# Kernel tuning notes

Hardware: AMD Instinct MI355X
Metric: run time of the kernel (lower is better)

The kernel has to match this reference:

```python
import jax, jax.numpy as jnp
import numpy as np

IN_CH, OUT_CH, K, STRIDE, PAD = 256, 256, 5, 1, 2


def setup_inputs() -> dict:
    key = jax.random.key(0)
    kx, kw = jax.random.split(key)
    x = jax.random.normal(kx, (32, IN_CH, 4096), dtype=jnp.float32)
    # kaiming_uniform_(a=sqrt(5)) -> bound = 1/sqrt(fan_in), fan_in = in_ch*k
    bound = 1.0 / np.sqrt(IN_CH * K)
    weight = jax.random.uniform(kw, (OUT_CH, IN_CH, K), dtype=jnp.float32,
                                minval=-bound, maxval=bound)
    bias = jnp.zeros((OUT_CH,), dtype=jnp.float32)
    return {"x": x, "weight": weight, "bias": bias}


def reference(x, weight, bias):
    # x: [B, C_in, W]; weight: [C_out, C_in, K] -> out: [B, C_out, W_out]
    out = jax.lax.conv_general_dilated(
        x, weight,
        window_strides=(STRIDE,),
        padding=[(PAD, PAD)],
        dimension_numbers=("NCH", "OIH", "NCH"),
    )
    return out + bias[None, :, None]
```

## Files before the change

kernel.cpp:

```cpp
#include <hip/hip_runtime.h>
#include <hip/hip_bf16.h>

typedef unsigned short u16;
typedef unsigned int u32;
typedef unsigned long long u64;
typedef __attribute__((ext_vector_type(8))) short short8;
typedef __attribute__((ext_vector_type(4))) float floatx4;

#define NB 32
#define NCI 256
#define NCO 256
#define NW 4096
#define NK 5

#define W3ROWB 80
#define W3TILE (256 * W3ROWB)
#define W3_BYTES (40 * W3TILE)

#define XROWB 64
#define XROWS 264
#define XBUF (XROWS * XROWB)

#define XSWZ(row) ((((row) >> 1) & 3) << 4)


__global__ void wprep(const float* __restrict__ wgt, u16* __restrict__ W3) {
    int i = blockIdx.x * 256 + threadIdx.x;
    if (i >= NCO * NCI * NK) return;
    int k  = i % NK;
    int ci = (i / NK) % NCI;
    int co = i / (NCI * NK);
    int cb = ci >> 5, cr = ci & 31;
    __hip_bfloat16 h = __float2bfloat16(wgt[i]);
    W3[((size_t)(cb * NK + k) * 256 + co) * 40 + cr] = *reinterpret_cast<u16*>(&h);
}

__device__ __forceinline__ u16 bf16bits(float f) {
    __hip_bfloat16 h = __float2bfloat16(f);
    return *reinterpret_cast<u16*>(&h);
}


__global__ __launch_bounds__(512, 2)
void conv_mfma(const float* __restrict__ x, const u16* __restrict__ W3,
               const float* __restrict__ bias, float* __restrict__ out) {
    __shared__ __align__(16) char xlds[2 * XBUF];

    const int bid  = blockIdx.x;
    const int wt   = bid & 15;
    const int b    = bid >> 4;
    const int tid  = threadIdx.x;
    const int lane = tid & 63;
    const int wave = tid >> 6;
    const int wm   = wave >> 2;
    const int wn   = wave & 3;
    const int mrow = lane & 15;
    const int g    = lane >> 4;
    const int w0   = wt * 256;

    floatx4 acc[8][4];
#pragma unroll
    for (int mi = 0; mi < 8; ++mi)
#pragma unroll
        for (int ni = 0; ni < 4; ++ni)
            acc[mi][ni] = (floatx4){0.f, 0.f, 0.f, 0.f};

    const float* xb = x + (size_t)b * NCI * NW;

    const int srow = tid & 255;
    const int h    = tid >> 8;
    char* const sdst0_base = xlds + (srow + 4) * XROWB + ((h * 32) ^ XSWZ(srow + 4));
    char* const sdst1_base = xlds + (srow + 4) * XROWB + ((h * 32 + 16) ^ XSWZ(srow + 4));

    const int hside = tid >> 5;
    const int hr    = (tid >> 3) & 3;
    const int hcq   = tid & 7;
    const int hrow  = hside ? (260 + hr) : hr;
    const int hwg   = hside ? (w0 + 256 + hr) : (w0 - 4 + hr);
    const bool hvalid = (hwg >= 0) && (hwg < NW);
    const int hoff  = hrow * XROWB + ((hcq * 8) ^ XSWZ(hrow));

    {
        float v[16];
        float hv[4] = {0.f, 0.f, 0.f, 0.f};
#pragma unroll
        for (int j = 0; j < 16; ++j)
            v[j] = xb[(size_t)(h * 16 + j) * NW + w0 + srow];
        if (tid < 64 && hvalid)
#pragma unroll
            for (int q = 0; q < 4; ++q)
                hv[q] = xb[(size_t)(hcq * 4 + q) * NW + hwg];

        u32 p[8];
#pragma unroll
        for (int j = 0; j < 8; ++j)
            p[j] = (u32)bf16bits(v[2 * j]) | ((u32)bf16bits(v[2 * j + 1]) << 16);
        *(int4*)sdst0_base = *(int4*)&p[0];
        *(int4*)sdst1_base = *(int4*)&p[4];
        if (tid < 64) {
            u64 hp = (u64)bf16bits(hv[0]) | ((u64)bf16bits(hv[1]) << 16) |
                     ((u64)bf16bits(hv[2]) << 32) | ((u64)bf16bits(hv[3]) << 48);
            *(u64*)(xlds + hoff) = hp;
        }
    }
    __syncthreads();

    for (int cb = 0; cb < 8; ++cb) {
        const char* cur = xlds + (cb & 1) * XBUF;
        char* nxt       = xlds + ((cb + 1) & 1) * XBUF;
        const bool more = (cb < 7);

        float v[16];
        float hv[4] = {0.f, 0.f, 0.f, 0.f};
        if (more) {
            const float* xcb = xb + (size_t)((cb + 1) * 32) * NW;
#pragma unroll
            for (int j = 0; j < 16; ++j)
                v[j] = xcb[(size_t)(h * 16 + j) * NW + w0 + srow];
            if (tid < 64 && hvalid)
#pragma unroll
                for (int q = 0; q < 4; ++q)
                    hv[q] = xcb[(size_t)(hcq * 4 + q) * NW + hwg];
        }

#pragma unroll
        for (int t = 0; t < NK; ++t) {
            const char* wtile = (const char*)W3 + (size_t)(cb * NK + t) * W3TILE;
            short8 af[8], bf[4];
#pragma unroll
            for (int mi = 0; mi < 8; ++mi)
                af[mi] = *(const short8*)(wtile +
                         (wm * 128 + mi * 16 + mrow) * W3ROWB + g * 16);
#pragma unroll
            for (int ni = 0; ni < 4; ++ni) {
                int rowx = wn * 64 + ni * 16 + mrow + t + 2;
                bf[ni] = *(const short8*)(cur + rowx * XROWB + ((g * 16) ^ XSWZ(rowx)));
            }

            __builtin_amdgcn_s_setprio(1);
#pragma unroll
            for (int mi = 0; mi < 8; ++mi)
#pragma unroll
                for (int ni = 0; ni < 4; ++ni)
                    acc[mi][ni] = __builtin_amdgcn_mfma_f32_16x16x32_bf16(
                        af[mi], bf[ni], acc[mi][ni], 0, 0, 0);
            __builtin_amdgcn_s_setprio(0);
        }

        if (more) {
            u32 p[8];
#pragma unroll
            for (int j = 0; j < 8; ++j)
                p[j] = (u32)bf16bits(v[2 * j]) | ((u32)bf16bits(v[2 * j + 1]) << 16);
            *(int4*)(nxt + (sdst0_base - xlds)) = *(int4*)&p[0];
            *(int4*)(nxt + (sdst1_base - xlds)) = *(int4*)&p[4];
            if (tid < 64) {
                u64 hp = (u64)bf16bits(hv[0]) | ((u64)bf16bits(hv[1]) << 16) |
                         ((u64)bf16bits(hv[2]) << 32) | ((u64)bf16bits(hv[3]) << 48);
                *(u64*)(nxt + hoff) = hp;
            }
            __syncthreads();
        }
    }

#pragma unroll
    for (int mi = 0; mi < 8; ++mi) {
        int cobase = wm * 128 + mi * 16 + g * 4;
        float bv[4];
#pragma unroll
        for (int r = 0; r < 4; ++r) bv[r] = bias[cobase + r];
#pragma unroll
        for (int ni = 0; ni < 4; ++ni) {
            int col = w0 + wn * 64 + ni * 16 + mrow;
#pragma unroll
            for (int r = 0; r < 4; ++r)
                out[((size_t)b * NCO + cobase + r) * NW + col] =
                    acc[mi][ni][r] + bv[r];
        }
    }
}


__global__ void conv_naive(const float* __restrict__ x, const float* __restrict__ wgt,
                           const float* __restrict__ bias, float* __restrict__ out) {
    int w  = blockIdx.x * 256 + threadIdx.x;
    int co = blockIdx.y;
    int b  = blockIdx.z;
    float acc = bias[co];
    for (int ci = 0; ci < NCI; ci++) {
        const float* xr = x + ((size_t)b * NCI + ci) * NW;
        const float* wr = wgt + ((size_t)co * NCI + ci) * NK;
#pragma unroll
        for (int k = 0; k < NK; k++) {
            int wi = w + k - 2;
            if (wi >= 0 && wi < NW) acc += xr[wi] * wr[k];
        }
    }
    out[((size_t)b * NCO + co) * NW + w] = acc;
}


extern "C" void kernel_launch(void* const* d_in, const int* in_sizes, int n_in,
                              void* d_out, int out_size, void* d_ws, size_t ws_size,
                              hipStream_t stream) {
    const float* x    = (const float*)d_in[0];
    const float* wgt  = (const float*)d_in[1];
    const float* bias = (const float*)d_in[2];
    float* out        = (float*)d_out;

    if (ws_size < (size_t)W3_BYTES) {
        conv_naive<<<dim3(NW / 256, NCO, NB), 256, 0, stream>>>(x, wgt, bias, out);
        return;
    }

    u16* W3 = (u16*)d_ws;
    wprep<<<(NCO * NCI * NK + 255) / 256, 256, 0, stream>>>(wgt, W3);
    conv_mfma<<<512, 512, 0, stream>>>(x, W3, bias, out);
}
```

Before: 109.6 us.

## Stage swizzled bf16 weight tiles into LDS via direct global-to-LDS loads

New measurement: 106.8 us. 1.03x faster.

```diff
diff --git a/kernel.cpp b/kernel.cpp
--- a/kernel.cpp
+++ b/kernel.cpp
@@ -13,9 +13,9 @@
 #define NW 4096
 #define NK 5
 
-#define W3ROWB 80
-#define W3TILE (256 * W3ROWB)
-#define W3_BYTES (40 * W3TILE)
+#define W4TILE 81920
+#define W4_BYTES (8 * W4TILE)
+#define WLDS W4TILE
 
 #define XROWB 64
 #define XROWS 264
@@ -24,15 +24,18 @@
 #define XSWZ(row) ((((row) >> 1) & 3) << 4)
 
 
-__global__ void wprep(const float* __restrict__ wgt, u16* __restrict__ W3) {
+__global__ void wprep(const float* __restrict__ wgt, u16* __restrict__ W4) {
     int i = blockIdx.x * 256 + threadIdx.x;
     if (i >= NCO * NCI * NK) return;
     int k  = i % NK;
     int ci = (i / NK) % NCI;
     int co = i / (NCI * NK);
     int cb = ci >> 5, cr = ci & 31;
+    int row  = k * 256 + co;
+    int slot = (cr >> 3) ^ (((row >> 1) & 3));
     __hip_bfloat16 h = __float2bfloat16(wgt[i]);
-    W3[((size_t)(cb * NK + k) * 256 + co) * 40 + cr] = *reinterpret_cast<u16*>(&h);
+    W4[(size_t)cb * (W4TILE / 2) + row * 32 + slot * 8 + (cr & 7)] =
+        *reinterpret_cast<u16*>(&h);
 }
 
 __device__ __forceinline__ u16 bf16bits(float f) {
@@ -40,11 +43,19 @@
     return *reinterpret_cast<u16*>(&h);
 }
 
+__device__ __forceinline__ void gload_lds16(const void* gsrc, void* ldst) {
+    __builtin_amdgcn_global_load_lds(
+        (const __attribute__((address_space(1))) unsigned int*)gsrc,
+        (__attribute__((address_space(3))) unsigned int*)ldst, 16, 0, 0);
+}
+
 
 __global__ __launch_bounds__(512, 2)
-void conv_mfma(const float* __restrict__ x, const u16* __restrict__ W3,
+void conv_mfma(const float* __restrict__ x, const u16* __restrict__ W4,
                const float* __restrict__ bias, float* __restrict__ out) {
-    __shared__ __align__(16) char xlds[2 * XBUF];
+    __shared__ __align__(16) char smem[WLDS + 2 * XBUF];
+    char* const wlds = smem;
+    char* const xlds = smem + WLDS;
 
     const int bid  = blockIdx.x;
     const int wt   = bid & 15;
@@ -66,11 +77,12 @@
             acc[mi][ni] = (floatx4){0.f, 0.f, 0.f, 0.f};
 
     const float* xb = x + (size_t)b * NCI * NW;
+    const char*  wimg = (const char*)W4;
 
     const int srow = tid & 255;
     const int h    = tid >> 8;
-    char* const sdst0_base = xlds + (srow + 4) * XROWB + ((h * 32) ^ XSWZ(srow + 4));
-    char* const sdst1_base = xlds + (srow + 4) * XROWB + ((h * 32 + 16) ^ XSWZ(srow + 4));
+    const int soff0 = (srow + 4) * XROWB + ((h * 32) ^ XSWZ(srow + 4));
+    const int soff1 = (srow + 4) * XROWB + ((h * 32 + 16) ^ XSWZ(srow + 4));
 
     const int hside = tid >> 5;
     const int hr    = (tid >> 3) & 3;
@@ -81,6 +93,11 @@
     const int hoff  = hrow * XROWB + ((hcq * 8) ^ XSWZ(hrow));
 
     {
+#pragma unroll
+        for (int k = 0; k < 10; ++k) {
+            int c = wave + 8 * k;
+            gload_lds16(wimg + c * 1024 + lane * 16, wlds + c * 1024);
+        }
         float v[16];
         float hv[4] = {0.f, 0.f, 0.f, 0.f};
 #pragma unroll
@@ -95,8 +112,8 @@
 #pragma unroll
         for (int j = 0; j < 8; ++j)
             p[j] = (u32)bf16bits(v[2 * j]) | ((u32)bf16bits(v[2 * j + 1]) << 16);
-        *(int4*)sdst0_base = *(int4*)&p[0];
-        *(int4*)sdst1_base = *(int4*)&p[4];
+        *(int4*)(xlds + soff0) = *(int4*)&p[0];
+        *(int4*)(xlds + soff1) = *(int4*)&p[4];
         if (tid < 64) {
             u64 hp = (u64)bf16bits(hv[0]) | ((u64)bf16bits(hv[1]) << 16) |
                      ((u64)bf16bits(hv[2]) << 32) | ((u64)bf16bits(hv[3]) << 48);
@@ -125,12 +142,12 @@
 
 #pragma unroll
         for (int t = 0; t < NK; ++t) {
-            const char* wtile = (const char*)W3 + (size_t)(cb * NK + t) * W3TILE;
             short8 af[8], bf[4];
 #pragma unroll
-            for (int mi = 0; mi < 8; ++mi)
-                af[mi] = *(const short8*)(wtile +
-                         (wm * 128 + mi * 16 + mrow) * W3ROWB + g * 16);
+            for (int mi = 0; mi < 8; ++mi) {
+                int roww = t * 256 + wm * 128 + mi * 16 + mrow;
+                af[mi] = *(const short8*)(wlds + roww * 64 + ((g * 16) ^ XSWZ(roww)));
+            }
 #pragma unroll
             for (int ni = 0; ni < 4; ++ni) {
                 int rowx = wn * 64 + ni * 16 + mrow + t + 2;
@@ -148,12 +165,21 @@
         }
 
         if (more) {
+            __syncthreads();
+
+#pragma unroll
+            for (int k = 0; k < 10; ++k) {
+                int c = wave + 8 * k;
+                gload_lds16(wimg + (size_t)(cb + 1) * W4TILE + c * 1024 + lane * 16,
+                            wlds + c * 1024);
+            }
+
             u32 p[8];
 #pragma unroll
             for (int j = 0; j < 8; ++j)
                 p[j] = (u32)bf16bits(v[2 * j]) | ((u32)bf16bits(v[2 * j + 1]) << 16);
-            *(int4*)(nxt + (sdst0_base - xlds)) = *(int4*)&p[0];
-            *(int4*)(nxt + (sdst1_base - xlds)) = *(int4*)&p[4];
+            *(int4*)(nxt + soff0) = *(int4*)&p[0];
+            *(int4*)(nxt + soff1) = *(int4*)&p[4];
             if (tid < 64) {
                 u64 hp = (u64)bf16bits(hv[0]) | ((u64)bf16bits(hv[1]) << 16) |
                          ((u64)bf16bits(hv[2]) << 32) | ((u64)bf16bits(hv[3]) << 48);
@@ -208,12 +234,12 @@
     const float* bias = (const float*)d_in[2];
     float* out        = (float*)d_out;
 
-    if (ws_size < (size_t)W3_BYTES) {
+    if (ws_size < (size_t)W4_BYTES) {
         conv_naive<<<dim3(NW / 256, NCO, NB), 256, 0, stream>>>(x, wgt, bias, out);
         return;
     }
 
-    u16* W3 = (u16*)d_ws;
-    wprep<<<(NCO * NCI * NK + 255) / 256, 256, 0, stream>>>(wgt, W3);
-    conv_mfma<<<512, 512, 0, stream>>>(x, W3, bias, out);
-}
+    u16* W4 = (u16*)d_ws;
+    wprep<<<(NCO * NCI * NK + 255) / 256, 256, 0, stream>>>(wgt, W4);
+    conv_mfma<<<512, 512, 0, stream>>>(x, W4, bias, out);
+}
```

## Stage weight tiles in LDS via async global_load_lds with per-tap double buffering

Applied to the files above, without the earlier changes.

New measurement: 95.60 us. -12.8%, faster.

```diff
diff --git a/kernel.cpp b/kernel.cpp
--- a/kernel.cpp
+++ b/kernel.cpp
@@ -3,7 +3,6 @@
 
 typedef unsigned short u16;
 typedef unsigned int u32;
-typedef unsigned long long u64;
 typedef __attribute__((ext_vector_type(8))) short short8;
 typedef __attribute__((ext_vector_type(4))) float floatx4;
 
@@ -13,26 +12,30 @@
 #define NW 4096
 #define NK 5
 
-#define W3ROWB 80
-#define W3TILE (256 * W3ROWB)
-#define W3_BYTES (40 * W3TILE)
+#define WSTEP 16384
+#define W2_BYTES (40 * WSTEP)
 
 #define XROWB 64
-#define XROWS 264
+#define XROWS 260
 #define XBUF (XROWS * XROWB)
-
-#define XSWZ(row) ((((row) >> 1) & 3) << 4)
-
-
-__global__ void wprep(const float* __restrict__ wgt, u16* __restrict__ W3) {
+#define XSWZ(r) ((((r) >> 1) & 3) << 4)
+
+#define FENCE asm volatile("" ::: "memory")
+#define VM0   asm volatile("s_waitcnt vmcnt(0)" ::: "memory")
+#define LK0   asm volatile("s_waitcnt lgkmcnt(0)" ::: "memory")
+
+
+__global__ void wprep(const float* __restrict__ wgt, u16* __restrict__ W2) {
     int i = blockIdx.x * 256 + threadIdx.x;
     if (i >= NCO * NCI * NK) return;
     int k  = i % NK;
     int ci = (i / NK) % NCI;
     int co = i / (NCI * NK);
     int cb = ci >> 5, cr = ci & 31;
+    int s    = cb * NK + k;
+    int slot = (cr >> 3) ^ ((co >> 1) & 3);
     __hip_bfloat16 h = __float2bfloat16(wgt[i]);
-    W3[((size_t)(cb * NK + k) * 256 + co) * 40 + cr] = *reinterpret_cast<u16*>(&h);
+    W2[(size_t)(s * 256 + co) * 32 + slot * 8 + (cr & 7)] = *reinterpret_cast<u16*>(&h);
 }
 
 __device__ __forceinline__ u16 bf16bits(float f) {
@@ -40,11 +43,19 @@
     return *reinterpret_cast<u16*>(&h);
 }
 
+__device__ __forceinline__ void gload_lds16(const void* gsrc, void* ldst) {
+    __builtin_amdgcn_global_load_lds(
+        (const __attribute__((address_space(1))) unsigned int*)gsrc,
+        (__attribute__((address_space(3))) unsigned int*)ldst, 16, 0, 0);
+}
+
 
 __global__ __launch_bounds__(512, 2)
-void conv_mfma(const float* __restrict__ x, const u16* __restrict__ W3,
+void conv_mfma(const float* __restrict__ x, const u16* __restrict__ W2,
                const float* __restrict__ bias, float* __restrict__ out) {
-    __shared__ __align__(16) char xlds[2 * XBUF];
+    __shared__ __align__(16) char smem[2 * WSTEP + 2 * XBUF];
+    char* const wlds = smem;
+    char* const xlds = smem + 2 * WSTEP;
 
     const int bid  = blockIdx.x;
     const int wt   = bid & 15;
@@ -65,78 +76,82 @@
         for (int ni = 0; ni < 4; ++ni)
             acc[mi][ni] = (floatx4){0.f, 0.f, 0.f, 0.f};
 
-    const float* xb = x + (size_t)b * NCI * NW;
-
-    const int srow = tid & 255;
+    const float* xb   = x + (size_t)b * NCI * NW;
+    const char*  wimg = (const char*)W2;
+
+    const int wloc = tid & 255;
     const int h    = tid >> 8;
-    char* const sdst0_base = xlds + (srow + 4) * XROWB + ((h * 32) ^ XSWZ(srow + 4));
-    char* const sdst1_base = xlds + (srow + 4) * XROWB + ((h * 32 + 16) ^ XSWZ(srow + 4));
-
-    const int hside = tid >> 5;
-    const int hr    = (tid >> 3) & 3;
-    const int hcq   = tid & 7;
-    const int hrow  = hside ? (260 + hr) : hr;
-    const int hwg   = hside ? (w0 + 256 + hr) : (w0 - 4 + hr);
-    const bool hvalid = (hwg >= 0) && (hwg < NW);
-    const int hoff  = hrow * XROWB + ((hcq * 8) ^ XSWZ(hrow));
+    const int soff0 = (2 + wloc) * XROWB + ((h * 32) ^ XSWZ(2 + wloc));
+    const int soff1 = (2 + wloc) * XROWB + ((h * 32 + 16) ^ XSWZ(2 + wloc));
+    const float* xcol = xb + w0 + wloc;
+
+    const int hidx = wave * 16 + (lane & 15);
+    const int hri  = hidx >> 5;
+    const int hci  = hidx & 31;
+    const int hwg  = (hri < 2) ? (w0 - 2 + hri) : (w0 + 256 + (hri - 2));
+    const int hwc  = (hwg < 0) ? 0 : ((hwg > NW - 1) ? (NW - 1) : hwg);
+    const bool hok = (hwg >= 0) && (hwg < NW);
+    const int hrloc = (hri < 2) ? hri : (258 + (hri - 2));
+    const int hoff  = hrloc * XROWB + (((hci >> 3) ^ ((hrloc >> 1) & 3)) * 16) + (hci & 7) * 2;
 
     {
+        gload_lds16(wimg + (wave * 2) * 1024 + lane * 16, wlds + (wave * 2) * 1024);
+        gload_lds16(wimg + (wave * 2 + 1) * 1024 + lane * 16, wlds + (wave * 2 + 1) * 1024);
         float v[16];
-        float hv[4] = {0.f, 0.f, 0.f, 0.f};
 #pragma unroll
         for (int j = 0; j < 16; ++j)
-            v[j] = xb[(size_t)(h * 16 + j) * NW + w0 + srow];
-        if (tid < 64 && hvalid)
-#pragma unroll
-            for (int q = 0; q < 4; ++q)
-                hv[q] = xb[(size_t)(hcq * 4 + q) * NW + hwg];
-
+            v[j] = xcol[(size_t)(h * 16 + j) * NW];
+        float hvv = xb[(size_t)hci * NW + hwc];
         u32 p[8];
 #pragma unroll
-        for (int j = 0; j < 8; ++j)
-            p[j] = (u32)bf16bits(v[2 * j]) | ((u32)bf16bits(v[2 * j + 1]) << 16);
-        *(int4*)sdst0_base = *(int4*)&p[0];
-        *(int4*)sdst1_base = *(int4*)&p[4];
-        if (tid < 64) {
-            u64 hp = (u64)bf16bits(hv[0]) | ((u64)bf16bits(hv[1]) << 16) |
-                     ((u64)bf16bits(hv[2]) << 32) | ((u64)bf16bits(hv[3]) << 48);
-            *(u64*)(xlds + hoff) = hp;
-        }
-    }
-    __syncthreads();
-
+        for (int jp = 0; jp < 8; ++jp)
+            p[jp] = (u32)bf16bits(v[2 * jp]) | ((u32)bf16bits(v[2 * jp + 1]) << 16);
+        *(int4*)(xlds + soff0) = *(int4*)&p[0];
+        *(int4*)(xlds + soff1) = *(int4*)&p[4];
+        if ((lane & 63) < 16)
+            *(u16*)(xlds + hoff) = bf16bits(hok ? hvv : 0.f);
+        LK0; VM0;
+    }
+    FENCE; __builtin_amdgcn_s_barrier(); FENCE;
+
+    float v[16];
+    float hvv = 0.f;
     for (int cb = 0; cb < 8; ++cb) {
-        const char* cur = xlds + (cb & 1) * XBUF;
-        char* nxt       = xlds + ((cb + 1) & 1) * XBUF;
-        const bool more = (cb < 7);
-
-        float v[16];
-        float hv[4] = {0.f, 0.f, 0.f, 0.f};
-        if (more) {
-            const float* xcb = xb + (size_t)((cb + 1) * 32) * NW;
-#pragma unroll
-            for (int j = 0; j < 16; ++j)
-                v[j] = xcb[(size_t)(h * 16 + j) * NW + w0 + srow];
-            if (tid < 64 && hvalid)
-#pragma unroll
-                for (int q = 0; q < 4; ++q)
-                    hv[q] = xcb[(size_t)(hcq * 4 + q) * NW + hwg];
-        }
-
+        const char* xcur = xlds + (cb & 1) * XBUF;
+        char* xnxt       = xlds + ((cb + 1) & 1) * XBUF;
+        const bool more  = (cb < 7);
 #pragma unroll
         for (int t = 0; t < NK; ++t) {
-            const char* wtile = (const char*)W3 + (size_t)(cb * NK + t) * W3TILE;
+            const int s = cb * NK + t;
+            if (s < 39) {
+                const char* src = wimg + (size_t)(s + 1) * WSTEP;
+                char* dst = wlds + ((s + 1) & 1) * WSTEP;
+                gload_lds16(src + (wave * 2) * 1024 + lane * 16, dst + (wave * 2) * 1024);
+                gload_lds16(src + (wave * 2 + 1) * 1024 + lane * 16, dst + (wave * 2 + 1) * 1024);
+            }
+            FENCE;
+            if (t < 4 && more) {
+                const float* sx = xcol + (size_t)((cb + 1) * 32 + h * 16 + t * 4) * NW;
+                v[t * 4 + 0] = sx[0];
+                v[t * 4 + 1] = sx[(size_t)NW];
+                v[t * 4 + 2] = sx[(size_t)2 * NW];
+                v[t * 4 + 3] = sx[(size_t)3 * NW];
+            }
+            if (t == 0 && more)
+                hvv = xb[(size_t)((cb + 1) * 32 + hci) * NW + hwc];
+            FENCE;
+            const char* wcur = wlds + (s & 1) * WSTEP;
             short8 af[8], bf[4];
 #pragma unroll
-            for (int mi = 0; mi < 8; ++mi)
-                af[mi] = *(const short8*)(wtile +
-                         (wm * 128 + mi * 16 + mrow) * W3ROWB + g * 16);
+            for (int mi = 0; mi < 8; ++mi) {
+                int rw = wm * 128 + mi * 16 + mrow;
+                af[mi] = *(const short8*)(wcur + rw * 64 + ((g * 16) ^ XSWZ(rw)));
+            }
 #pragma unroll
             for (int ni = 0; ni < 4; ++ni) {
-                int rowx = wn * 64 + ni * 16 + mrow + t + 2;
-                bf[ni] = *(const short8*)(cur + rowx * XROWB + ((g * 16) ^ XSWZ(rowx)));
-            }
-
+                int rx = wn * 64 + ni * 16 + mrow + t;
+                bf[ni] = *(const short8*)(xcur + rx * XROWB + ((g * 16) ^ XSWZ(rx)));
+            }
             __builtin_amdgcn_s_setprio(1);
 #pragma unroll
             for (int mi = 0; mi < 8; ++mi)
@@ -145,21 +160,18 @@
                     acc[mi][ni] = __builtin_amdgcn_mfma_f32_16x16x32_bf16(
                         af[mi], bf[ni], acc[mi][ni], 0, 0, 0);
             __builtin_amdgcn_s_setprio(0);
-        }
-
-        if (more) {
-            u32 p[8];
-#pragma unroll
-            for (int j = 0; j < 8; ++j)
-                p[j] = (u32)bf16bits(v[2 * j]) | ((u32)bf16bits(v[2 * j + 1]) << 16);
-            *(int4*)(nxt + (sdst0_base - xlds)) = *(int4*)&p[0];
-            *(int4*)(nxt + (sdst1_base - xlds)) = *(int4*)&p[4];
-            if (tid < 64) {
-                u64 hp = (u64)bf16bits(hv[0]) | ((u64)bf16bits(hv[1]) << 16) |
-                         ((u64)bf16bits(hv[2]) << 32) | ((u64)bf16bits(hv[3]) << 48);
-                *(u64*)(nxt + hoff) = hp;
-            }
-            __syncthreads();
+            if (t == 4 && more) {
+                u32 p[8];
+#pragma unroll
+                for (int jp = 0; jp < 8; ++jp)
+                    p[jp] = (u32)bf16bits(v[2 * jp]) | ((u32)bf16bits(v[2 * jp + 1]) << 16);
+                *(int4*)(xnxt + soff0) = *(int4*)&p[0];
+                *(int4*)(xnxt + soff1) = *(int4*)&p[4];
+                if ((lane & 63) < 16)
+                    *(u16*)(xnxt + hoff) = bf16bits(hok ? hvv : 0.f);
+            }
+            LK0; VM0;
+            FENCE; __builtin_amdgcn_s_barrier(); FENCE;
         }
     }
 
@@ -208,12 +220,12 @@
     const float* bias = (const float*)d_in[2];
     float* out        = (float*)d_out;
 
-    if (ws_size < (size_t)W3_BYTES) {
+    if (ws_size < (size_t)W2_BYTES) {
         conv_naive<<<dim3(NW / 256, NCO, NB), 256, 0, stream>>>(x, wgt, bias, out);
         return;
     }
 
-    u16* W3 = (u16*)d_ws;
-    wprep<<<(NCO * NCI * NK + 255) / 256, 256, 0, stream>>>(wgt, W3);
-    conv_mfma<<<512, 512, 0, stream>>>(x, W3, bias, out);
-}
+    u16* W2 = (u16*)d_ws;
+    wprep<<<(NCO * NCI * NK + 255) / 256, 256, 0, stream>>>(wgt, W2);
+    conv_mfma<<<512, 512, 0, stream>>>(x, W2, bias, out);
+}
```
